# Kernel optimization log

Measured on AMD Instinct MI355X. Metric: run time of the kernel, lower is better.

The kernel has to match this reference:

```python
import jax, jax.numpy as jnp
import numpy as np

B, S, D = 32, 1024, 256
F_, K = 256, 3
T = 8192
LN_EPS = 1e-5


def _conv1d(x, w, b, padding):
    # x: [B, S, C_in], w: [C_out, C_in, K] -> [B, S, C_out]
    y = jax.lax.conv_general_dilated(
        x.transpose(0, 2, 1), w, window_strides=(1,),
        padding=[(padding, padding)], dimension_numbers=('NCH', 'OIH', 'NCH'))
    return y.transpose(0, 2, 1) + b


def _layernorm(x, g, b):
    mu = jnp.mean(x, axis=-1, keepdims=True)
    var = jnp.mean(jnp.square(x - mu), axis=-1, keepdims=True)
    return (x - mu) * jax.lax.rsqrt(var + LN_EPS) * g + b


def setup_inputs() -> dict:
    key = jax.random.key(0)
    ks = jax.random.split(key, 8)
    sc = 0.02
    return {
        'x': jax.random.normal(ks[0], (B, S, D), dtype=jnp.float32),
        'mask': jnp.zeros((B, S), dtype=bool),
        'duration': jax.random.randint(ks[1], (B, S), 0, 8, dtype=jnp.int32),
        'max_len': T,
        'conv1_w': jax.random.normal(ks[2], (F_, D, K), dtype=jnp.float32) * sc,
        'conv1_b': jnp.zeros((F_,), dtype=jnp.float32),
        'ln1_g': jnp.ones((F_,), dtype=jnp.float32),
        'ln1_b': jnp.zeros((F_,), dtype=jnp.float32),
        'conv2_w': jax.random.normal(ks[3], (F_, F_, K), dtype=jnp.float32) * sc,
        'conv2_b': jnp.zeros((F_,), dtype=jnp.float32),
        'ln2_g': jnp.ones((F_,), dtype=jnp.float32),
        'ln2_b': jnp.zeros((F_,), dtype=jnp.float32),
        'lin_w': jax.random.normal(ks[4], (F_, 1), dtype=jnp.float32) * sc,
        'lin_b': jnp.zeros((1,), dtype=jnp.float32),
    }


def reference(x, mask, duration, max_len, conv1_w, conv1_b, ln1_g, ln1_b,
              conv2_w, conv2_b, ln2_g, ln2_b, lin_w, lin_b):
    # ---- duration predictor (eval mode: dropout = identity) ----
    h = _conv1d(x, conv1_w, conv1_b, (K - 1) // 2)
    h = _layernorm(jax.nn.relu(h), ln1_g, ln1_b)
    h = _conv1d(h, conv2_w, conv2_b, 1)
    h = _layernorm(jax.nn.relu(h), ln2_g, ln2_b)
    log_dur = (h @ lin_w + lin_b)[..., 0]  # [B, S]
    log_dur = jnp.where(mask, 0.0, log_dur)

    # ---- length regulator: repeat_interleave + pad, done as one gather ----
    dur = duration.astype(jnp.int32)
    cum = jnp.cumsum(dur, axis=1)                                   # [B, S]
    t = jnp.arange(max_len, dtype=jnp.int32)                        # [T]
    src_idx = jax.vmap(lambda c: jnp.searchsorted(c, t, side='right'))(cum)  # [B, T]
    mel_len = jnp.minimum(cum[:, -1], max_len)                      # [B]
    valid = t[None, :] < mel_len[:, None]                           # [B, T]
    src_idx = jnp.clip(src_idx, 0, x.shape[1] - 1)
    out = jnp.take_along_axis(x, src_idx[:, :, None], axis=1)       # [B, T, D]
    out = jnp.where(valid[:, :, None], out, 0.0)
    # duration_target path -> duration_rounded = duration, mel_mask stays None
    return out, log_dur, dur, mel_len
```

## Files before the change

kernel.cpp:

```cpp
#include <hip/hip_runtime.h>
#include <cstddef>

constexpr int Bb   = 32;
constexpr int Ss   = 1024;
constexpr int Dd   = 256;
constexpr int Ff   = 256;
constexpr int TMAX = 8192;
constexpr int MM   = Bb * Ss;
constexpr int KK   = 768;
constexpr int SP   = 1026;
constexpr float LN_EPS = 1e-5f;
constexpr int PIT  = 72;

constexpr int GEMM_BLK = MM / 64;
constexpr int GATH_TOT = Bb * TMAX * Dd / 4 / 256;
constexpr int GATH_HALF = GATH_TOT / 2;

typedef __bf16 bf16x8 __attribute__((ext_vector_type(8)));
typedef __bf16 bf16x4 __attribute__((ext_vector_type(4)));
typedef float  f32x4  __attribute__((ext_vector_type(4)));

__global__ __launch_bounds__(256) void prep_k(
    const float* __restrict__ w1, const float* __restrict__ w2,
    __bf16* __restrict__ wTT1, __bf16* __restrict__ wTT2,
    const int* __restrict__ dur, float* __restrict__ dur_out,
    float* __restrict__ mel_out, int* __restrict__ idx,
    __bf16* __restrict__ xp2)
{
    __shared__ int ic[1024];
    __shared__ int sc[256];
    const int blk = blockIdx.x;
    const int tid = threadIdx.x;

    if (blk < 1536) {
        int i = blk * 256 + tid;
        const float* w = w1;
        __bf16* o = wTT1;
        int j = i;
        if (j >= Ff * KK) { j -= Ff * KK; w = w2; o = wTT2; }
        int d  = j & 255;
        int fk = j >> 8;
        int f  = fk / 3;
        int k  = fk - f * 3;
        o[(size_t)f * KK + k * 256 + d] = (__bf16)w[((size_t)(f * 256 + d)) * 3 + k];
        return;
    }
    if (blk >= 1568) {
        int j = (blk - 1568) * 256 + tid;
        int b = j >> 7;
        int r = (j >> 6) & 1;
        int d = (j & 63) * 4;
        *(bf16x4*)&xp2[((size_t)b * SP + (size_t)r * (SP - 1)) * 256 + d] =
            (bf16x4)(__bf16)0.f;
        return;
    }
    int b = blk - 1536;
    int4 d4 = ((const int4*)(dur + b * 1024))[tid];
    int l0 = d4.x, l1 = l0 + d4.y, l2 = l1 + d4.z, l3 = l2 + d4.w;
    sc[tid] = l3;
    __syncthreads();
    for (int off = 1; off < 256; off <<= 1) {
        int v = (tid >= off) ? sc[tid - off] : 0;
        __syncthreads();
        sc[tid] += v;
        __syncthreads();
    }
    int excl = sc[tid] - l3;
    ((int4*)ic)[tid] = make_int4(excl + l0, excl + l1, excl + l2, excl + l3);
    ((float4*)(dur_out + b * 1024))[tid] =
        make_float4((float)d4.x, (float)d4.y, (float)d4.z, (float)d4.w);
    if (tid == 255) mel_out[b] = (float)min(excl + l3, TMAX);
    __syncthreads();
    int mel = min(ic[1023], TMAX);
    for (int t = tid; t < TMAX; t += 256) {
        int lo = 0, hi = 1024;
        #pragma unroll
        for (int it = 0; it < 10; ++it) {
            int mid = (lo + hi) >> 1;
            if (ic[mid] <= t) lo = mid + 1; else hi = mid;
        }
        idx[b * TMAX + t] = (t < mel) ? min(lo, 1023) : -1;
    }
}

template<int MODE>
__global__ __launch_bounds__(256, 3) void gemm_fused(
    const float* __restrict__ Xf,
    const __bf16* __restrict__ Ap,
    const __bf16* __restrict__ Bw,
    const float* __restrict__ bias,
    const float* __restrict__ g, const float* __restrict__ bt,
    const float* __restrict__ lw, const float* __restrict__ lb,
    const unsigned char* __restrict__ mask,
    __bf16* __restrict__ outB, float* __restrict__ outF,
    const int* __restrict__ idx, float4* __restrict__ outv)
{
    __shared__ __bf16 As[64 * PIT];
    __shared__ __bf16 Bs[256 * PIT];

    const int tid = threadIdx.x;

    if (blockIdx.x >= GEMM_BLK) {
        int gblk = blockIdx.x - GEMM_BLK + MODE * GATH_HALF;
        int gg   = gblk * 256 + tid;
        int row  = gg >> 6;
        int col  = gg & 63;
        int s = idx[row];
        float4 v = make_float4(0.f, 0.f, 0.f, 0.f);
        if (s >= 0) {
            int b = row >> 13;
            v = ((const float4*)Xf)[((size_t)(b << 10) + s) * 64 + col];
        }
        outv[gg] = v;
        return;
    }

    const int m0   = blockIdx.x * 64;
    const int bb   = m0 >> 10;
    const int s0   = m0 & 1023;
    const int wave = tid >> 6;
    const int lane = tid & 63;
    const int wn   = wave * 64;
    const int lm   = lane & 15;
    const int lk   = lane >> 4;

    f32x4 acc[4][4] = {};

    for (int step = 0; step < KK / 64; ++step) {
        const int kk0  = step * 64;
        const int kblk = kk0 >> 8;
        const int d0   = kk0 & 255;

        if constexpr (MODE == 0) {
            #pragma unroll
            for (int i = 0; i < 4; ++i) {
                int c = i * 256 + tid;
                int r = c >> 4, q = c & 15;
                int sg = s0 + r + kblk - 1;
                bf16x4 o = (bf16x4)(__bf16)0.f;
                if ((unsigned)sg < 1024u) {
                    float4 v = *(const float4*)&Xf[
                        (((size_t)(bb << 10) + sg) << 8) + d0 + q * 4];
                    o[0] = (__bf16)v.x; o[1] = (__bf16)v.y;
                    o[2] = (__bf16)v.z; o[3] = (__bf16)v.w;
                }
                *(bf16x4*)&As[r * PIT + q * 4] = o;
            }
        } else {
            const __bf16* aSrc = Ap + (((size_t)(bb * SP + s0 + kblk)) << 8) + d0;
            #pragma unroll
            for (int i = 0; i < 2; ++i) {
                int c = i * 256 + tid, r = c >> 3, q = c & 7;
                *(bf16x8*)&As[r * PIT + q * 8] =
                    *(const bf16x8*)&aSrc[((size_t)r << 8) + q * 8];
            }
        }
        const __bf16* bSrc = Bw + kk0;
        #pragma unroll
        for (int i = 0; i < 8; ++i) {
            int c = i * 256 + tid, r = c >> 3, q = c & 7;
            *(bf16x8*)&Bs[r * PIT + q * 8] =
                *(const bf16x8*)&bSrc[(size_t)r * KK + q * 8];
        }
        __syncthreads();
        #pragma unroll
        for (int kc = 0; kc < 2; ++kc) {
            bf16x8 af[4], bfr[4];
            #pragma unroll
            for (int mi = 0; mi < 4; ++mi)
                af[mi] = *(const bf16x8*)&As[(mi * 16 + lm) * PIT + kc * 32 + lk * 8];
            #pragma unroll
            for (int ni = 0; ni < 4; ++ni)
                bfr[ni] = *(const bf16x8*)&Bs[(wn + ni * 16 + lm) * PIT + kc * 32 + lk * 8];
            #pragma unroll
            for (int mi = 0; mi < 4; ++mi)
                #pragma unroll
                for (int ni = 0; ni < 4; ++ni)
                    acc[mi][ni] = __builtin_amdgcn_mfma_f32_16x16x32_bf16(
                        af[mi], bfr[ni], acc[mi][ni], 0, 0, 0);
        }
        __syncthreads();
    }

    float* scrS = (float*)As;
    float* scrQ = scrS + 256;

    float s_[4][4] = {}, q_[4][4] = {};
    #pragma unroll
    for (int ni = 0; ni < 4; ++ni) {
        float bv = bias[wn + ni * 16 + lm];
        #pragma unroll
        for (int mi = 0; mi < 4; ++mi)
            #pragma unroll
            for (int r = 0; r < 4; ++r) {
                float h = fmaxf(acc[mi][ni][r] + bv, 0.f);
                acc[mi][ni][r] = h;
                s_[mi][r] += h;
                q_[mi][r] += h * h;
            }
    }
    #pragma unroll
    for (int off = 1; off < 16; off <<= 1)
        #pragma unroll
        for (int mi = 0; mi < 4; ++mi)
            #pragma unroll
            for (int r = 0; r < 4; ++r) {
                s_[mi][r] += __shfl_xor(s_[mi][r], off, 64);
                q_[mi][r] += __shfl_xor(q_[mi][r], off, 64);
            }
    if (lm == 0) {
        #pragma unroll
        for (int mi = 0; mi < 4; ++mi)
            #pragma unroll
            for (int r = 0; r < 4; ++r) {
                int row = mi * 16 + lk * 4 + r;
                scrS[wave * 64 + row] = s_[mi][r];
                scrQ[wave * 64 + row] = q_[mi][r];
            }
    }
    __syncthreads();

    float mu[4][4], rs[4][4];
    #pragma unroll
    for (int mi = 0; mi < 4; ++mi)
        #pragma unroll
        for (int r = 0; r < 4; ++r) {
            int row = mi * 16 + lk * 4 + r;
            float S = scrS[row] + scrS[64 + row] + scrS[128 + row] + scrS[192 + row];
            float Q = scrQ[row] + scrQ[64 + row] + scrQ[128 + row] + scrQ[192 + row];
            float m_ = S * (1.f / 256.f);
            float v_ = Q * (1.f / 256.f) - m_ * m_;
            mu[mi][r] = m_;
            rs[mi][r] = rsqrtf(v_ + LN_EPS);
        }

    if constexpr (MODE == 0) {
        size_t obase = ((size_t)(bb * SP + s0 + 1)) << 8;
        #pragma unroll
        for (int ni = 0; ni < 4; ++ni) {
            int col = wn + ni * 16 + lm;
            float gv = g[col], bv2 = bt[col];
            #pragma unroll
            for (int mi = 0; mi < 4; ++mi)
                #pragma unroll
                for (int r = 0; r < 4; ++r) {
                    int row = mi * 16 + lk * 4 + r;
                    float o = (acc[mi][ni][r] - mu[mi][r]) * rs[mi][r] * gv + bv2;
                    outB[obase + ((size_t)row << 8) + col] = (__bf16)o;
                }
        }
    } else {
        float p_[4][4] = {};
        #pragma unroll
        for (int ni = 0; ni < 4; ++ni) {
            int col = wn + ni * 16 + lm;
            float gv = g[col], bv2 = bt[col], wv = lw[col];
            #pragma unroll
            for (int mi = 0; mi < 4; ++mi)
                #pragma unroll
                for (int r = 0; r < 4; ++r) {
                    float o = (acc[mi][ni][r] - mu[mi][r]) * rs[mi][r] * gv + bv2;
                    p_[mi][r] += o * wv;
                }
        }
        #pragma unroll
        for (int off = 1; off < 16; off <<= 1)
            #pragma unroll
            for (int mi = 0; mi < 4; ++mi)
                #pragma unroll
                for (int r = 0; r < 4; ++r)
                    p_[mi][r] += __shfl_xor(p_[mi][r], off, 64);
        __syncthreads();
        if (lm == 0) {
            #pragma unroll
            for (int mi = 0; mi < 4; ++mi)
                #pragma unroll
                for (int r = 0; r < 4; ++r)
                    scrS[wave * 64 + (mi * 16 + lk * 4 + r)] = p_[mi][r];
        }
        __syncthreads();
        if (tid < 64) {
            int row = tid;
            float v = scrS[row] + scrS[64 + row] + scrS[128 + row] + scrS[192 + row]
                      + lb[0];
            if (mask[m0 + row]) v = 0.f;
            outF[m0 + row] = v;
        }
    }
}

extern "C" void kernel_launch(void* const* d_in, const int* in_sizes, int n_in,
                              void* d_out, int out_size, void* d_ws, size_t ws_size,
                              hipStream_t stream)
{
    const float* x            = (const float*)d_in[0];
    const unsigned char* mask = (const unsigned char*)d_in[1];
    const int* duration       = (const int*)d_in[2];
    const float* w1  = (const float*)d_in[4];
    const float* b1  = (const float*)d_in[5];
    const float* g1  = (const float*)d_in[6];
    const float* be1 = (const float*)d_in[7];
    const float* w2  = (const float*)d_in[8];
    const float* b2  = (const float*)d_in[9];
    const float* g2  = (const float*)d_in[10];
    const float* be2 = (const float*)d_in[11];
    const float* lw  = (const float*)d_in[12];
    const float* lb  = (const float*)d_in[13];

    float* out        = (float*)d_out;
    float* out0       = out;
    float* out_logdur = out + (size_t)Bb * TMAX * Dd;
    float* out_dur    = out_logdur + (size_t)Bb * Ss;
    float* out_mel    = out_dur + (size_t)Bb * Ss;

    char* ws = (char*)d_ws;
    __bf16* xp2  = (__bf16*)ws;
    __bf16* wTT1 = xp2 + (size_t)Bb * SP * 256;
    __bf16* wTT2 = wTT1 + (size_t)Ff * KK;
    int*    idx  = (int*)(wTT2 + (size_t)Ff * KK);

    prep_k<<<1584, 256, 0, stream>>>(w1, w2, wTT1, wTT2,
                                     duration, out_dur, out_mel, idx, xp2);
    gemm_fused<0><<<GEMM_BLK + GATH_HALF, 256, 0, stream>>>(
        x, nullptr, wTT1, b1, g1, be1, nullptr, nullptr, nullptr,
        xp2, nullptr, idx, (float4*)out0);
    gemm_fused<1><<<GEMM_BLK + GATH_HALF, 256, 0, stream>>>(
        x, xp2, wTT2, b2, g2, be2, lw, lb, mask,
        nullptr, out_logdur, idx, (float4*)out0);
}
```

Before: 388.2 us.

## Batch gather rider blocks with nontemporal stores and stage conv1 output through LDS

The gather blocks that ride along each GEMM launch now copy 16 float4s per thread: all index loads are issued first, then all source loads, then nontemporal stores. This cuts the gather block count 16-fold and keeps the 256MB output stream from polluting cache. The MODE 0 epilogue now writes the LayerNorm output into an LDS tile (reusing the B buffer with a wider pitch) and emits coalesced 16-byte bf16 stores, replacing scattered 2-byte global stores. The cost is more registers per gather thread, which may lower occupancy, plus an extra barrier in the epilogue.

```diff
diff --git a/kernel.cpp b/kernel.cpp
--- a/kernel.cpp
+++ b/kernel.cpp
@@ -11,10 +11,11 @@
 constexpr int SP   = 1026;
 constexpr float LN_EPS = 1e-5f;
 constexpr int PIT  = 72;
-
-constexpr int GEMM_BLK = MM / 64;
-constexpr int GATH_TOT = Bb * TMAX * Dd / 4 / 256;
-constexpr int GATH_HALF = GATH_TOT / 2;
+constexpr int OPIT = 264;
+
+constexpr int GEMM_BLK  = MM / 64;
+constexpr int RIDER_PER = 2048;
+constexpr int RIDER_F4  = 4096;
 
 typedef __bf16 bf16x8 __attribute__((ext_vector_type(8)));
 typedef __bf16 bf16x4 __attribute__((ext_vector_type(4)));
@@ -93,25 +94,38 @@
     const float* __restrict__ lw, const float* __restrict__ lb,
     const unsigned char* __restrict__ mask,
     __bf16* __restrict__ outB, float* __restrict__ outF,
-    const int* __restrict__ idx, float4* __restrict__ outv)
+    const int* __restrict__ idx, f32x4* __restrict__ outv)
 {
     __shared__ __bf16 As[64 * PIT];
-    __shared__ __bf16 Bs[256 * PIT];
+    __shared__ __bf16 Bs[64 * OPIT];
+    __shared__ __bf16 Bs2[256 * PIT - 64 * OPIT];
 
     const int tid = threadIdx.x;
 
     if (blockIdx.x >= GEMM_BLK) {
-        int gblk = blockIdx.x - GEMM_BLK + MODE * GATH_HALF;
-        int gg   = gblk * 256 + tid;
-        int row  = gg >> 6;
-        int col  = gg & 63;
-        int s = idx[row];
-        float4 v = make_float4(0.f, 0.f, 0.f, 0.f);
-        if (s >= 0) {
-            int b = row >> 13;
-            v = ((const float4*)Xf)[((size_t)(b << 10) + s) * 64 + col];
-        }
-        outv[gg] = v;
+        int rblk = blockIdx.x - GEMM_BLK + MODE * RIDER_PER;
+        size_t base = (size_t)rblk * RIDER_F4 + tid;
+        int sarr[16];
+        #pragma unroll
+        for (int it = 0; it < 16; ++it) {
+            size_t gg = base + (size_t)it * 256;
+            sarr[it] = idx[gg >> 6];
+        }
+        f32x4 v[16];
+        #pragma unroll
+        for (int it = 0; it < 16; ++it) {
+            size_t gg = base + (size_t)it * 256;
+            int row = (int)(gg >> 6);
+            int col = (int)(gg & 63);
+            v[it] = (f32x4)0.f;
+            if (sarr[it] >= 0) {
+                int b = row >> 13;
+                v[it] = ((const f32x4*)Xf)[((size_t)(b << 10) + sarr[it]) * 64 + col];
+            }
+        }
+        #pragma unroll
+        for (int it = 0; it < 16; ++it)
+            __builtin_nontemporal_store(v[it], &outv[base + (size_t)it * 256]);
         return;
     }
 
@@ -123,6 +137,8 @@
     const int wn   = wave * 64;
     const int lm   = lane & 15;
     const int lk   = lane >> 4;
+
+    __bf16* BsK = Bs;
 
     f32x4 acc[4][4] = {};
 
@@ -159,7 +175,7 @@
         #pragma unroll
         for (int i = 0; i < 8; ++i) {
             int c = i * 256 + tid, r = c >> 3, q = c & 7;
-            *(bf16x8*)&Bs[r * PIT + q * 8] =
+            *(bf16x8*)&BsK[r * PIT + q * 8] =
                 *(const bf16x8*)&bSrc[(size_t)r * KK + q * 8];
         }
         __syncthreads();
@@ -171,7 +187,7 @@
                 af[mi] = *(const bf16x8*)&As[(mi * 16 + lm) * PIT + kc * 32 + lk * 8];
             #pragma unroll
             for (int ni = 0; ni < 4; ++ni)
-                bfr[ni] = *(const bf16x8*)&Bs[(wn + ni * 16 + lm) * PIT + kc * 32 + lk * 8];
+                bfr[ni] = *(const bf16x8*)&BsK[(wn + ni * 16 + lm) * PIT + kc * 32 + lk * 8];
             #pragma unroll
             for (int mi = 0; mi < 4; ++mi)
                 #pragma unroll
@@ -235,7 +251,7 @@
         }
 
     if constexpr (MODE == 0) {
-        size_t obase = ((size_t)(bb * SP + s0 + 1)) << 8;
+        __bf16* tile = Bs;
         #pragma unroll
         for (int ni = 0; ni < 4; ++ni) {
             int col = wn + ni * 16 + lm;
@@ -246,8 +262,17 @@
                 for (int r = 0; r < 4; ++r) {
                     int row = mi * 16 + lk * 4 + r;
                     float o = (acc[mi][ni][r] - mu[mi][r]) * rs[mi][r] * gv + bv2;
-                    outB[obase + ((size_t)row << 8) + col] = (__bf16)o;
+                    tile[row * OPIT + col] = (__bf16)o;
                 }
+        }
+        __syncthreads();
+        size_t obase = ((size_t)(bb * SP + s0 + 1)) << 8;
+        #pragma unroll
+        for (int i = 0; i < 8; ++i) {
+            int c = i * 256 + tid;
+            int row = c >> 5, q = c & 31;
+            *(bf16x8*)&outB[obase + ((size_t)row << 8) + q * 8] =
+                *(bf16x8*)&tile[row * OPIT + q * 8];
         }
     } else {
         float p_[4][4] = {};
@@ -321,10 +346,10 @@
 
     prep_k<<<1584, 256, 0, stream>>>(w1, w2, wTT1, wTT2,
                                      duration, out_dur, out_mel, idx, xp2);
-    gemm_fused<0><<<GEMM_BLK + GATH_HALF, 256, 0, stream>>>(
+    gemm_fused<0><<<GEMM_BLK + RIDER_PER, 256, 0, stream>>>(
         x, nullptr, wTT1, b1, g1, be1, nullptr, nullptr, nullptr,
-        xp2, nullptr, idx, (float4*)out0);
-    gemm_fused<1><<<GEMM_BLK + GATH_HALF, 256, 0, stream>>>(
+        xp2, nullptr, idx, (f32x4*)out0);
+    gemm_fused<1><<<GEMM_BLK + RIDER_PER, 256, 0, stream>>>(
         x, xp2, wTT2, b2, g2, be2, lw, lb, mask,
-        nullptr, out_logdur, idx, (float4*)out0);
+        nullptr, out_logdur, idx, (f32x4*)out0);
 }
```

Measured after the change: 356.2 us. 8.2% less time.
